# Optimization experiments

Hardware: AMD Instinct MI355X
Metric: run time of the kernel (lower is better)

Reference implementation:

```python
import jax, jax.numpy as jnp
import numpy as np

D_MODEL = 512
N_HEADS = 8
D_HEAD = D_MODEL // N_HEADS
EPS = 1e-5  # torch LayerNorm default


def setup_inputs() -> dict:
    key = jax.random.key(0)
    ks = jax.random.split(key, 10)
    s = 0.02
    return {
        "x": jax.random.normal(ks[0], (4, 2048, D_MODEL), dtype=jnp.float32),
        "wq": jax.random.normal(ks[1], (D_MODEL, D_MODEL), dtype=jnp.float32) * s,
        "bq": jnp.zeros((D_MODEL,), jnp.float32),
        "wk": jax.random.normal(ks[2], (D_MODEL, D_MODEL), dtype=jnp.float32) * s,
        "bk": jnp.zeros((D_MODEL,), jnp.float32),
        "wv": jax.random.normal(ks[3], (D_MODEL, D_MODEL), dtype=jnp.float32) * s,
        "bv": jnp.zeros((D_MODEL,), jnp.float32),
        "wo": jax.random.normal(ks[4], (D_MODEL, D_MODEL), dtype=jnp.float32) * s,
        "bo": jnp.zeros((D_MODEL,), jnp.float32),
        "gamma": jnp.ones((D_MODEL,), jnp.float32),
        "beta": jnp.zeros((D_MODEL,), jnp.float32),
    }


def _attn(x, wq, bq, wk, bk, wv, bv, wo, bo, gamma, beta):
    B, S, D = x.shape
    residual = x
    # pre-norm LayerNorm
    mu = jnp.mean(x, axis=-1, keepdims=True)
    var = jnp.mean(jnp.square(x - mu), axis=-1, keepdims=True)
    xn = (x - mu) * jax.lax.rsqrt(var + EPS) * gamma + beta
    # QKV projections -> [B, H, S, d]
    q = (xn @ wq + bq).reshape(B, S, N_HEADS, D_HEAD).transpose(0, 2, 1, 3)
    k = (xn @ wk + bk).reshape(B, S, N_HEADS, D_HEAD).transpose(0, 2, 1, 3)
    v = (xn @ wv + bv).reshape(B, S, N_HEADS, D_HEAD).transpose(0, 2, 1, 3)
    scale = D_HEAD ** -0.5
    scores = jnp.einsum("bhqd,bhkd->bhqk", q, k) * scale  # full S x S matrix
    attn = jax.nn.softmax(scores, axis=-1)  # dropout off (eval)
    out = jnp.einsum("bhqk,bhkd->bhqd", attn, v)
    out = out.transpose(0, 2, 1, 3).reshape(B, S, D)
    out = out @ wo + bo
    return out + residual


def reference(x, wq, bq, wk, bk, wv, bv, wo, bo, gamma, beta):
    return _attn(x, wq, bq, wk, bk, wv, bv, wo, bo, gamma, beta)
```

## Files before the change

### kernel.cpp

```cpp
#include <hip/hip_runtime.h>
#include <hip/hip_bf16.h>

#define D_MODEL 512
#define N_HEADS 8
#define D_HEAD  64
#define SEQ     2048
#define BATCH   4
#define ROWS    (BATCH * SEQ)
#define EPS     1e-5f
#define SCALE   0.125f

typedef __attribute__((ext_vector_type(8))) short short8;
typedef __attribute__((ext_vector_type(4))) float f32x4;

__device__ __forceinline__ unsigned short f2bf(float f) {
  return __builtin_bit_cast(unsigned short, __float2bfloat16(f));
}

__global__ __launch_bounds__(128) void ln_kernel(const float* __restrict__ x,
                                                 const float* __restrict__ gamma,
                                                 const float* __restrict__ beta,
                                                 unsigned short* __restrict__ xn) {
  const int row = blockIdx.x;
  const int t   = threadIdx.x;
  const float4 v = ((const float4*)(x + (size_t)row * D_MODEL))[t];
  float s  = v.x + v.y + v.z + v.w;
  float s2 = v.x*v.x + v.y*v.y + v.z*v.z + v.w*v.w;
#pragma unroll
  for (int o = 32; o > 0; o >>= 1) {
    s  += __shfl_down(s,  o, 64);
    s2 += __shfl_down(s2, o, 64);
  }
  __shared__ float ps[2], ps2[2];
  if ((t & 63) == 0) { ps[t >> 6] = s; ps2[t >> 6] = s2; }
  __syncthreads();
  s  = ps[0] + ps[1];
  s2 = ps2[0] + ps2[1];
  const float mu  = s * (1.0f / D_MODEL);
  const float var = s2 * (1.0f / D_MODEL) - mu * mu;
  const float rs  = rsqrtf(var + EPS);
  const float4 g = ((const float4*)gamma)[t];
  const float4 b = ((const float4*)beta)[t];
  ushort4 o;
  o.x = f2bf((v.x - mu) * rs * g.x + b.x);
  o.y = f2bf((v.y - mu) * rs * g.y + b.y);
  o.z = f2bf((v.z - mu) * rs * g.z + b.z);
  o.w = f2bf((v.w - mu) * rs * g.w + b.w);
  ((ushort4*)(xn + (size_t)row * D_MODEL))[t] = o;
}

__device__ __forceinline__ void bf16_gemm_tile(const unsigned short* __restrict__ A,
                                               const float* __restrict__ W,
                                               unsigned short (&Wt)[64 * 40],
                                               f32x4 (&acc)[4],
                                               int bm, int bn) {
  const int tid  = threadIdx.x;
  const int lane = tid & 63;
  const int l4   = lane & 15;
  const int lg   = lane >> 4;
  const int wv   = tid >> 6;

  short8 af[16];
  const unsigned short* ap = A + (size_t)(bm * 64 + wv * 16 + l4) * D_MODEL + lg * 8;
#pragma unroll
  for (int kt = 0; kt < 16; kt++)
    af[kt] = *(const short8*)(ap + kt * 32);

  const int wk  = tid >> 3;
  const int wn0 = (tid & 7) * 8;

  for (int kt = 0; kt < 16; kt++) {
    const float* wp = W + (size_t)(kt * 32 + wk) * D_MODEL + bn * 64 + wn0;
    const float4 f0 = *(const float4*)wp;
    const float4 f1 = *(const float4*)(wp + 4);
    const float vals[8] = {f0.x, f0.y, f0.z, f0.w, f1.x, f1.y, f1.z, f1.w};
    __syncthreads();
#pragma unroll
    for (int i = 0; i < 8; i++)
      Wt[(wn0 + i) * 40 + wk] = f2bf(vals[i]);
    __syncthreads();
#pragma unroll
    for (int nt = 0; nt < 4; nt++) {
      const short8 b = *(const short8*)&Wt[(nt * 16 + l4) * 40 + lg * 8];
      acc[nt] = __builtin_amdgcn_mfma_f32_16x16x32_bf16(af[kt], b, acc[nt], 0, 0, 0);
    }
  }
}

__global__ __launch_bounds__(256) void qkv_mfma_kernel(const unsigned short* __restrict__ xn,
                                                       const float* __restrict__ wq, const float* __restrict__ bq,
                                                       const float* __restrict__ wk, const float* __restrict__ bk,
                                                       const float* __restrict__ wv, const float* __restrict__ bv,
                                                       unsigned short* __restrict__ qo,
                                                       unsigned short* __restrict__ ko,
                                                       unsigned short* __restrict__ vo) {
  __shared__ __align__(16) unsigned short Wt[64 * 40];
  const float* W; const float* bias; unsigned short* out; float scale;
  switch (blockIdx.z) {
    case 0:  W = wq; bias = bq; out = qo; scale = SCALE; break;
    case 1:  W = wk; bias = bk; out = ko; scale = 1.0f;  break;
    default: W = wv; bias = bv; out = vo; scale = 1.0f;  break;
  }
  f32x4 acc[4];
#pragma unroll
  for (int i = 0; i < 4; i++) acc[i] = (f32x4){0.f, 0.f, 0.f, 0.f};
  bf16_gemm_tile(xn, W, Wt, acc, blockIdx.x, blockIdx.y);

  const int lane = threadIdx.x & 63, wv_ = threadIdx.x >> 6;
  const int l4 = lane & 15, lg = lane >> 4;
  const int h = blockIdx.y;
#pragma unroll
  for (int nt = 0; nt < 4; nt++) {
    const float bb = bias[h * 64 + nt * 16 + l4];
#pragma unroll
    for (int r = 0; r < 4; r++) {
      const int row = blockIdx.x * 64 + wv_ * 16 + lg * 4 + r;
      const int b_  = row >> 11;
      const int s   = row & (SEQ - 1);
      out[((size_t)(b_ * N_HEADS + h) * SEQ + s) * D_HEAD + nt * 16 + l4] =
          f2bf((acc[nt][r] + bb) * scale);
    }
  }
}

__global__ __launch_bounds__(256) void attn_mfma_kernel(const unsigned short* __restrict__ q,
                                                        const unsigned short* __restrict__ k,
                                                        const unsigned short* __restrict__ v,
                                                        unsigned short* __restrict__ att) {
  __shared__ __align__(16) unsigned short K_lds[32 * 64];
  __shared__ __align__(16) unsigned short Vt_lds[64 * 40];
  __shared__ __align__(16) unsigned short P_lds[4][16 * 40];

  const int tid  = threadIdx.x;
  const int lane = tid & 63;
  const int w    = tid >> 6;
  const int l4   = lane & 15;
  const int lg   = lane >> 4;

  const int swz = (blockIdx.x & 7) * 128 + (blockIdx.x >> 3);
  const int qb  = swz & 31;
  const int bh  = swz >> 5;

  const unsigned short* qbase = q + (size_t)bh * SEQ * D_HEAD;
  const unsigned short* kbase = k + (size_t)bh * SEQ * D_HEAD;
  const unsigned short* vbase = v + (size_t)bh * SEQ * D_HEAD;

  short8 aq[2];
  {
    const unsigned short* qp = qbase + (size_t)(qb * 64 + w * 16 + l4) * D_HEAD + lg * 8;
    aq[0] = *(const short8*)(qp);
    aq[1] = *(const short8*)(qp + 32);
  }

  f32x4 o[4];
#pragma unroll
  for (int i = 0; i < 4; i++) o[i] = (f32x4){0.f, 0.f, 0.f, 0.f};
  float m_[4] = {-1e30f, -1e30f, -1e30f, -1e30f};
  float l_[4] = {0.f, 0.f, 0.f, 0.f};

  const int kj   = tid >> 3;
  const int kg   = tid & 7;
  const int kswz = kg ^ (kj & 7);
  const int vj   = tid & 31;
  const int vd0  = (tid >> 5) * 8;

  for (int t = 0; t < SEQ / 32; t++) {
    const int kv0 = t * 32;
    {
      const short8 pk = *(const short8*)(kbase + (size_t)(kv0 + kj) * D_HEAD + kg * 8);
      *(short8*)&K_lds[kj * 64 + kswz * 8] = pk;
    }
    {
      const short8 vv = *(const short8*)(vbase + (size_t)(kv0 + vj) * D_HEAD + vd0);
#pragma unroll
      for (int i = 0; i < 8; i++)
        Vt_lds[(vd0 + i) * 40 + vj] = (unsigned short)vv[i];
    }
    __syncthreads();

    f32x4 s[2];
#pragma unroll
    for (int kt2 = 0; kt2 < 2; kt2++) {
      const int krow = kt2 * 16 + l4;
      f32x4 acc = (f32x4){0.f, 0.f, 0.f, 0.f};
#pragma unroll
      for (int dt = 0; dt < 2; dt++) {
        const int g = (lg + dt * 4) ^ (krow & 7);
        const short8 bk = *(const short8*)&K_lds[krow * 64 + g * 8];
        acc = __builtin_amdgcn_mfma_f32_16x16x32_bf16(aq[dt], bk, acc, 0, 0, 0);
      }
      s[kt2] = acc;
    }

#pragma unroll
    for (int r = 0; r < 4; r++) {
      float mt = fmaxf(s[0][r], s[1][r]);
#pragma unroll
      for (int mask = 1; mask <= 8; mask <<= 1)
        mt = fmaxf(mt, __shfl_xor(mt, mask, 64));
      const float mn   = fmaxf(m_[r], mt);
      const float corr = __expf(m_[r] - mn);
      const float p0 = __expf(s[0][r] - mn);
      const float p1 = __expf(s[1][r] - mn);
      float rs = p0 + p1;
#pragma unroll
      for (int mask = 1; mask <= 8; mask <<= 1)
        rs += __shfl_xor(rs, mask, 64);
      l_[r] = l_[r] * corr + rs;
      m_[r] = mn;
      o[0][r] *= corr; o[1][r] *= corr; o[2][r] *= corr; o[3][r] *= corr;
      const int qr = lg * 4 + r;
      P_lds[w][qr * 40 + l4]      = f2bf(p0);
      P_lds[w][qr * 40 + 16 + l4] = f2bf(p1);
    }
    asm volatile("s_waitcnt lgkmcnt(0)" ::: "memory");
    __builtin_amdgcn_sched_barrier(0);

    const short8 pa = *(const short8*)&P_lds[w][l4 * 40 + lg * 8];
#pragma unroll
    for (int dtile = 0; dtile < 4; dtile++) {
      const short8 bv = *(const short8*)&Vt_lds[(dtile * 16 + l4) * 40 + lg * 8];
      o[dtile] = __builtin_amdgcn_mfma_f32_16x16x32_bf16(pa, bv, o[dtile], 0, 0, 0);
    }
    __syncthreads();
  }

  const int b_ = bh >> 3, h = bh & 7;
#pragma unroll
  for (int r = 0; r < 4; r++) {
    const int qrow = qb * 64 + w * 16 + lg * 4 + r;
    const float inv = 1.0f / l_[r];
    unsigned short* op = att + ((size_t)(b_ * SEQ + qrow)) * D_MODEL + h * D_HEAD;
#pragma unroll
    for (int dtile = 0; dtile < 4; dtile++)
      op[dtile * 16 + l4] = f2bf(o[dtile][r] * inv);
  }
}

__global__ __launch_bounds__(256) void proj_mfma_kernel(const unsigned short* __restrict__ att,
                                                        const float* __restrict__ wo,
                                                        const float* __restrict__ bo,
                                                        const float* __restrict__ x,
                                                        float* __restrict__ out) {
  __shared__ __align__(16) unsigned short Wt[64 * 40];
  f32x4 acc[4];
#pragma unroll
  for (int i = 0; i < 4; i++) acc[i] = (f32x4){0.f, 0.f, 0.f, 0.f};
  bf16_gemm_tile(att, wo, Wt, acc, blockIdx.x, blockIdx.y);

  const int lane = threadIdx.x & 63, wv_ = threadIdx.x >> 6;
  const int l4 = lane & 15, lg = lane >> 4;
#pragma unroll
  for (int nt = 0; nt < 4; nt++) {
    const float bb = bo[blockIdx.y * 64 + nt * 16 + l4];
#pragma unroll
    for (int r = 0; r < 4; r++) {
      const int row = blockIdx.x * 64 + wv_ * 16 + lg * 4 + r;
      const size_t off = (size_t)row * D_MODEL + blockIdx.y * 64 + nt * 16 + l4;
      out[off] = acc[nt][r] + bb + x[off];
    }
  }
}

extern "C" void kernel_launch(void* const* d_in, const int* in_sizes, int n_in,
                              void* d_out, int out_size, void* d_ws, size_t ws_size,
                              hipStream_t stream) {
  const float* x     = (const float*)d_in[0];
  const float* wq    = (const float*)d_in[1];
  const float* bq    = (const float*)d_in[2];
  const float* wk    = (const float*)d_in[3];
  const float* bk    = (const float*)d_in[4];
  const float* wv    = (const float*)d_in[5];
  const float* bv    = (const float*)d_in[6];
  const float* wo    = (const float*)d_in[7];
  const float* bo    = (const float*)d_in[8];
  const float* gamma = (const float*)d_in[9];
  const float* beta  = (const float*)d_in[10];
  float* out = (float*)d_out;

  unsigned short* xn  = (unsigned short*)d_ws;
  unsigned short* q   = xn + (size_t)ROWS * D_MODEL;
  unsigned short* k   = q  + (size_t)ROWS * D_MODEL;
  unsigned short* v   = k  + (size_t)ROWS * D_MODEL;
  unsigned short* att = xn;

  ln_kernel<<<ROWS, 128, 0, stream>>>(x, gamma, beta, xn);
  qkv_mfma_kernel<<<dim3(ROWS / 64, N_HEADS, 3), 256, 0, stream>>>(
      xn, wq, bq, wk, bk, wv, bv, q, k, v);
  attn_mfma_kernel<<<1024, 256, 0, stream>>>(q, k, v, att);
  proj_mfma_kernel<<<dim3(ROWS / 64, D_MODEL / 64), 256, 0, stream>>>(att, wo, bo, x, out);
}
```

Baseline: 348.1 us.

## Pre-transpose weights to bf16 and stream K from registers in attention

Adds a kernel that converts and transposes all four weight matrices to bf16 once per call. The QKV and output-projection GEMMs then read B fragments straight from global memory, with no LDS staging and no barriers. The attention kernel now processes 64-key tiles and reads K fragments directly into registers, prefetching the next tile while softmax runs. It only stages V through LDS and raises wave priority around the MFMAs. This cuts LDS traffic and synchronisation at the cost of extra workspace and a small extra launch, and it uncoalesced-ish global fragment loads rely on cache hits.

```diff
diff --git a/kernel.cpp b/kernel.cpp
--- a/kernel.cpp
+++ b/kernel.cpp
@@ -15,6 +15,40 @@
 
 __device__ __forceinline__ unsigned short f2bf(float f) {
   return __builtin_bit_cast(unsigned short, __float2bfloat16(f));
+}
+
+__global__ __launch_bounds__(256) void wtrans_kernel(const float* __restrict__ wq,
+                                                     const float* __restrict__ wk,
+                                                     const float* __restrict__ wv,
+                                                     const float* __restrict__ wo,
+                                                     unsigned short* __restrict__ wt) {
+  __shared__ float T[64][68];
+  const float* src;
+  switch (blockIdx.z) { case 0: src = wq; break; case 1: src = wk; break;
+                        case 2: src = wv; break; default: src = wo; }
+  const int tid = threadIdx.x;
+  const int bk = blockIdx.x, bn = blockIdx.y;
+  {
+    const int k = tid >> 2, n0 = (tid & 3) * 16;
+#pragma unroll
+    for (int j = 0; j < 4; j++) {
+      const float4 f = *(const float4*)(src + (size_t)(bk * 64 + k) * D_MODEL + bn * 64 + n0 + j * 4);
+      *(float4*)&T[k][n0 + j * 4] = f;
+    }
+  }
+  __syncthreads();
+  {
+    const int n = tid >> 2, k0 = (tid & 3) * 16;
+    short8 t0, t1;
+#pragma unroll
+    for (int j = 0; j < 8; j++) t0[j] = (short)f2bf(T[k0 + j][n]);
+#pragma unroll
+    for (int j = 0; j < 8; j++) t1[j] = (short)f2bf(T[k0 + 8 + j][n]);
+    unsigned short* dst = wt + (size_t)blockIdx.z * D_MODEL * D_MODEL
+                             + (size_t)(bn * 64 + n) * D_MODEL + bk * 64 + k0;
+    *(short8*)dst = t0;
+    *(short8*)(dst + 8) = t1;
+  }
 }
 
 __global__ __launch_bounds__(128) void ln_kernel(const float* __restrict__ x,
@@ -49,62 +83,44 @@
   ((ushort4*)(xn + (size_t)row * D_MODEL))[t] = o;
 }
 
-__device__ __forceinline__ void bf16_gemm_tile(const unsigned short* __restrict__ A,
-                                               const float* __restrict__ W,
-                                               unsigned short (&Wt)[64 * 40],
-                                               f32x4 (&acc)[4],
-                                               int bm, int bn) {
-  const int tid  = threadIdx.x;
-  const int lane = tid & 63;
-  const int l4   = lane & 15;
-  const int lg   = lane >> 4;
-  const int wv   = tid >> 6;
-
+__device__ __forceinline__ void bf16_gemm_global(const unsigned short* __restrict__ A,
+                                                 const unsigned short* __restrict__ Wt,
+                                                 f32x4 (&acc)[4], int bm, int bn) {
+  const int tid = threadIdx.x, lane = tid & 63;
+  const int l4 = lane & 15, lg = lane >> 4, wv_ = tid >> 6;
   short8 af[16];
-  const unsigned short* ap = A + (size_t)(bm * 64 + wv * 16 + l4) * D_MODEL + lg * 8;
-#pragma unroll
-  for (int kt = 0; kt < 16; kt++)
-    af[kt] = *(const short8*)(ap + kt * 32);
-
-  const int wk  = tid >> 3;
-  const int wn0 = (tid & 7) * 8;
-
+  const unsigned short* ap = A + (size_t)(bm * 64 + wv_ * 16 + l4) * D_MODEL + lg * 8;
+#pragma unroll
+  for (int kt = 0; kt < 16; kt++) af[kt] = *(const short8*)(ap + kt * 32);
+  const unsigned short* bp = Wt + (size_t)(bn * 64 + l4) * D_MODEL + lg * 8;
+#pragma unroll
   for (int kt = 0; kt < 16; kt++) {
-    const float* wp = W + (size_t)(kt * 32 + wk) * D_MODEL + bn * 64 + wn0;
-    const float4 f0 = *(const float4*)wp;
-    const float4 f1 = *(const float4*)(wp + 4);
-    const float vals[8] = {f0.x, f0.y, f0.z, f0.w, f1.x, f1.y, f1.z, f1.w};
-    __syncthreads();
-#pragma unroll
-    for (int i = 0; i < 8; i++)
-      Wt[(wn0 + i) * 40 + wk] = f2bf(vals[i]);
-    __syncthreads();
 #pragma unroll
     for (int nt = 0; nt < 4; nt++) {
-      const short8 b = *(const short8*)&Wt[(nt * 16 + l4) * 40 + lg * 8];
+      const short8 b = *(const short8*)(bp + (size_t)nt * 16 * D_MODEL + kt * 32);
       acc[nt] = __builtin_amdgcn_mfma_f32_16x16x32_bf16(af[kt], b, acc[nt], 0, 0, 0);
     }
   }
 }
 
 __global__ __launch_bounds__(256) void qkv_mfma_kernel(const unsigned short* __restrict__ xn,
-                                                       const float* __restrict__ wq, const float* __restrict__ bq,
-                                                       const float* __restrict__ wk, const float* __restrict__ bk,
-                                                       const float* __restrict__ wv, const float* __restrict__ bv,
+                                                       const unsigned short* __restrict__ wt,
+                                                       const float* __restrict__ bq,
+                                                       const float* __restrict__ bk_,
+                                                       const float* __restrict__ bv_,
                                                        unsigned short* __restrict__ qo,
                                                        unsigned short* __restrict__ ko,
                                                        unsigned short* __restrict__ vo) {
-  __shared__ __align__(16) unsigned short Wt[64 * 40];
-  const float* W; const float* bias; unsigned short* out; float scale;
-  switch (blockIdx.z) {
-    case 0:  W = wq; bias = bq; out = qo; scale = SCALE; break;
-    case 1:  W = wk; bias = bk; out = ko; scale = 1.0f;  break;
-    default: W = wv; bias = bv; out = vo; scale = 1.0f;  break;
-  }
+  const int z = blockIdx.z;
+  const unsigned short* W = wt + (size_t)z * D_MODEL * D_MODEL;
+  const float* bias = (z == 0) ? bq : ((z == 1) ? bk_ : bv_);
+  unsigned short* out = (z == 0) ? qo : ((z == 1) ? ko : vo);
+  const float scale = (z == 0) ? SCALE : 1.0f;
+
   f32x4 acc[4];
 #pragma unroll
   for (int i = 0; i < 4; i++) acc[i] = (f32x4){0.f, 0.f, 0.f, 0.f};
-  bf16_gemm_tile(xn, W, Wt, acc, blockIdx.x, blockIdx.y);
+  bf16_gemm_global(xn, W, acc, blockIdx.x, blockIdx.y);
 
   const int lane = threadIdx.x & 63, wv_ = threadIdx.x >> 6;
   const int l4 = lane & 15, lg = lane >> 4;
@@ -127,9 +143,8 @@
                                                         const unsigned short* __restrict__ k,
                                                         const unsigned short* __restrict__ v,
                                                         unsigned short* __restrict__ att) {
-  __shared__ __align__(16) unsigned short K_lds[32 * 64];
-  __shared__ __align__(16) unsigned short Vt_lds[64 * 40];
-  __shared__ __align__(16) unsigned short P_lds[4][16 * 40];
+  __shared__ __align__(16) unsigned short Vt_lds[64 * 72];
+  __shared__ __align__(16) unsigned short P_lds[4][16 * 72];
 
   const int tid  = threadIdx.x;
   const int lane = tid & 63;
@@ -158,51 +173,64 @@
   float m_[4] = {-1e30f, -1e30f, -1e30f, -1e30f};
   float l_[4] = {0.f, 0.f, 0.f, 0.f};
 
-  const int kj   = tid >> 3;
-  const int kg   = tid & 7;
-  const int kswz = kg ^ (kj & 7);
-  const int vj   = tid & 31;
-  const int vd0  = (tid >> 5) * 8;
-
-  for (int t = 0; t < SEQ / 32; t++) {
-    const int kv0 = t * 32;
+  const int vj  = tid & 63;
+  const int vd0 = (tid >> 6) * 16;
+
+  short8 kf[8];
+  short8 vf[2];
+#pragma unroll
+  for (int kt2 = 0; kt2 < 4; kt2++)
+#pragma unroll
+    for (int dt = 0; dt < 2; dt++)
+      kf[kt2 * 2 + dt] = *(const short8*)(kbase + (size_t)(kt2 * 16 + l4) * D_HEAD + dt * 32 + lg * 8);
+  vf[0] = *(const short8*)(vbase + (size_t)vj * D_HEAD + vd0);
+  vf[1] = *(const short8*)(vbase + (size_t)vj * D_HEAD + vd0 + 8);
+
+  for (int t = 0; t < SEQ / 64; t++) {
+    __syncthreads();
     {
-      const short8 pk = *(const short8*)(kbase + (size_t)(kv0 + kj) * D_HEAD + kg * 8);
-      *(short8*)&K_lds[kj * 64 + kswz * 8] = pk;
-    }
-    {
-      const short8 vv = *(const short8*)(vbase + (size_t)(kv0 + vj) * D_HEAD + vd0);
-#pragma unroll
-      for (int i = 0; i < 8; i++)
-        Vt_lds[(vd0 + i) * 40 + vj] = (unsigned short)vv[i];
+#pragma unroll
+      for (int i = 0; i < 2; i++)
+#pragma unroll
+        for (int e = 0; e < 8; e++)
+          Vt_lds[(vd0 + i * 8 + e) * 72 + vj] = (unsigned short)vf[i][e];
     }
     __syncthreads();
 
-    f32x4 s[2];
-#pragma unroll
-    for (int kt2 = 0; kt2 < 2; kt2++) {
-      const int krow = kt2 * 16 + l4;
+    f32x4 s[4];
+    __builtin_amdgcn_s_setprio(1);
+#pragma unroll
+    for (int kt2 = 0; kt2 < 4; kt2++) {
       f32x4 acc = (f32x4){0.f, 0.f, 0.f, 0.f};
-#pragma unroll
-      for (int dt = 0; dt < 2; dt++) {
-        const int g = (lg + dt * 4) ^ (krow & 7);
-        const short8 bk = *(const short8*)&K_lds[krow * 64 + g * 8];
-        acc = __builtin_amdgcn_mfma_f32_16x16x32_bf16(aq[dt], bk, acc, 0, 0, 0);
-      }
+      acc = __builtin_amdgcn_mfma_f32_16x16x32_bf16(aq[0], kf[kt2 * 2 + 0], acc, 0, 0, 0);
+      acc = __builtin_amdgcn_mfma_f32_16x16x32_bf16(aq[1], kf[kt2 * 2 + 1], acc, 0, 0, 0);
       s[kt2] = acc;
     }
+    __builtin_amdgcn_s_setprio(0);
+
+    if (t < SEQ / 64 - 1) {
+      const int kv0n = (t + 1) * 64;
+#pragma unroll
+      for (int kt2 = 0; kt2 < 4; kt2++)
+#pragma unroll
+        for (int dt = 0; dt < 2; dt++)
+          kf[kt2 * 2 + dt] = *(const short8*)(kbase + (size_t)(kv0n + kt2 * 16 + l4) * D_HEAD + dt * 32 + lg * 8);
+      vf[0] = *(const short8*)(vbase + (size_t)(kv0n + vj) * D_HEAD + vd0);
+      vf[1] = *(const short8*)(vbase + (size_t)(kv0n + vj) * D_HEAD + vd0 + 8);
+    }
 
 #pragma unroll
     for (int r = 0; r < 4; r++) {
-      float mt = fmaxf(s[0][r], s[1][r]);
+      float mt = fmaxf(fmaxf(s[0][r], s[1][r]), fmaxf(s[2][r], s[3][r]));
 #pragma unroll
       for (int mask = 1; mask <= 8; mask <<= 1)
         mt = fmaxf(mt, __shfl_xor(mt, mask, 64));
       const float mn   = fmaxf(m_[r], mt);
       const float corr = __expf(m_[r] - mn);
-      const float p0 = __expf(s[0][r] - mn);
-      const float p1 = __expf(s[1][r] - mn);
-      float rs = p0 + p1;
+      float p[4];
+      float rs = 0.f;
+#pragma unroll
+      for (int kt2 = 0; kt2 < 4; kt2++) { p[kt2] = __expf(s[kt2][r] - mn); rs += p[kt2]; }
 #pragma unroll
       for (int mask = 1; mask <= 8; mask <<= 1)
         rs += __shfl_xor(rs, mask, 64);
@@ -210,19 +238,24 @@
       m_[r] = mn;
       o[0][r] *= corr; o[1][r] *= corr; o[2][r] *= corr; o[3][r] *= corr;
       const int qr = lg * 4 + r;
-      P_lds[w][qr * 40 + l4]      = f2bf(p0);
-      P_lds[w][qr * 40 + 16 + l4] = f2bf(p1);
+#pragma unroll
+      for (int kt2 = 0; kt2 < 4; kt2++)
+        P_lds[w][qr * 72 + kt2 * 16 + l4] = f2bf(p[kt2]);
     }
     asm volatile("s_waitcnt lgkmcnt(0)" ::: "memory");
     __builtin_amdgcn_sched_barrier(0);
 
-    const short8 pa = *(const short8*)&P_lds[w][l4 * 40 + lg * 8];
+    const short8 pa0 = *(const short8*)&P_lds[w][l4 * 72 + lg * 8];
+    const short8 pa1 = *(const short8*)&P_lds[w][l4 * 72 + 32 + lg * 8];
+    __builtin_amdgcn_s_setprio(1);
 #pragma unroll
     for (int dtile = 0; dtile < 4; dtile++) {
-      const short8 bv = *(const short8*)&Vt_lds[(dtile * 16 + l4) * 40 + lg * 8];
-      o[dtile] = __builtin_amdgcn_mfma_f32_16x16x32_bf16(pa, bv, o[dtile], 0, 0, 0);
-    }
-    __syncthreads();
+      const short8 bv0 = *(const short8*)&Vt_lds[(dtile * 16 + l4) * 72 + lg * 8];
+      const short8 bv1 = *(const short8*)&Vt_lds[(dtile * 16 + l4) * 72 + 32 + lg * 8];
+      o[dtile] = __builtin_amdgcn_mfma_f32_16x16x32_bf16(pa0, bv0, o[dtile], 0, 0, 0);
+      o[dtile] = __builtin_amdgcn_mfma_f32_16x16x32_bf16(pa1, bv1, o[dtile], 0, 0, 0);
+    }
+    __builtin_amdgcn_s_setprio(0);
   }
 
   const int b_ = bh >> 3, h = bh & 7;
@@ -238,15 +271,14 @@
 }
 
 __global__ __launch_bounds__(256) void proj_mfma_kernel(const unsigned short* __restrict__ att,
-                                                        const float* __restrict__ wo,
+                                                        const unsigned short* __restrict__ wot,
                                                         const float* __restrict__ bo,
                                                         const float* __restrict__ x,
                                                         float* __restrict__ out) {
-  __shared__ __align__(16) unsigned short Wt[64 * 40];
   f32x4 acc[4];
 #pragma unroll
   for (int i = 0; i < 4; i++) acc[i] = (f32x4){0.f, 0.f, 0.f, 0.f};
-  bf16_gemm_tile(att, wo, Wt, acc, blockIdx.x, blockIdx.y);
+  bf16_gemm_global(att, wot, acc, blockIdx.x, blockIdx.y);
 
   const int lane = threadIdx.x & 63, wv_ = threadIdx.x >> 6;
   const int l4 = lane & 15, lg = lane >> 4;
@@ -282,11 +314,14 @@
   unsigned short* q   = xn + (size_t)ROWS * D_MODEL;
   unsigned short* k   = q  + (size_t)ROWS * D_MODEL;
   unsigned short* v   = k  + (size_t)ROWS * D_MODEL;
+  unsigned short* wt  = v  + (size_t)ROWS * D_MODEL;
   unsigned short* att = xn;
 
+  wtrans_kernel<<<dim3(8, 8, 4), 256, 0, stream>>>(wq, wk, wv, wo, wt);
   ln_kernel<<<ROWS, 128, 0, stream>>>(x, gamma, beta, xn);
   qkv_mfma_kernel<<<dim3(ROWS / 64, N_HEADS, 3), 256, 0, stream>>>(
-      xn, wq, bq, wk, bk, wv, bv, q, k, v);
+      xn, wt, bq, bk, bv, q, k, v);
   attn_mfma_kernel<<<1024, 256, 0, stream>>>(q, k, v, att);
-  proj_mfma_kernel<<<dim3(ROWS / 64, D_MODEL / 64), 256, 0, stream>>>(att, wo, bo, x, out);
-}
+  proj_mfma_kernel<<<dim3(ROWS / 64, D_MODEL / 64), 256, 0, stream>>>(
+      att, wt + (size_t)3 * D_MODEL * D_MODEL, bo, x, out);
+}
```

New measurement: 388.9 us. 11.7% more time.
